# Kernel tuning notes

Measured on AMD Instinct MI355X. Metric: run time of the kernel, lower is better.

## Reference

```python
import jax, jax.numpy as jnp
import numpy as np
from jax import lax

B, T, H, W, E = 64, 8, 8, 8, 512
REC = 2048


def setup_inputs() -> dict:
    key = jax.random.key(0)
    kx, kwi, kwr = jax.random.split(key, 3)
    x = jax.random.normal(kx, (B, T, H, W, E), dtype=jnp.float32)
    W_input = jax.random.normal(kwi, (E, REC), dtype=jnp.float32) / np.sqrt(E)
    W_recurrent = jax.random.normal(kwr, (REC, REC), dtype=jnp.float32) / np.sqrt(REC)
    return {"x": x, "W_input": W_input, "W_recurrent": W_recurrent}


def reference(x, W_input, W_recurrent):
    b, t, h, w, e = x.shape
    R = t * h * w
    rec = W_recurrent.shape[0]
    k = int(rec * 0.4)  # 819, matches torch: int(recurrent_size * 0.4)
    x_seq = jnp.swapaxes(x.reshape(b, R, e), 0, 1)  # [R, B, E]
    row_idx = jnp.arange(b)[:, None]

    def step(r, inp):
        z = r @ W_recurrent                    # [B, REC]
        vals, idx = lax.top_k(z, k)            # [B, k]
        s = jnp.zeros_like(z).at[row_idx, idx].set(vals)  # scatter top-k back
        r_new = jnp.tanh(inp @ W_input + s)
        r_new = r_new / (jnp.linalg.norm(r_new, axis=-1, keepdims=True) + 1e-6)
        return r_new, None

    r0 = jnp.zeros((b, rec), dtype=x.dtype)
    r_final, _ = lax.scan(step, r0, x_seq)
    return r_final
```

## Files before the change

### kernel.cpp

```cpp
#include <hip/hip_runtime.h>

#define NSTEP 512
#define EDIM  512
#define REC   2048
#define NB    64
#define KSEL  819
#define KC    8
#define ZCH   256
#define AP    264
#define CSTR  16896
#define WITC  1048576

typedef unsigned short u16;
typedef __bf16 bf16x8 __attribute__((ext_vector_type(8)));
typedef float  f32x4  __attribute__((ext_vector_type(4)));
typedef unsigned long long ull;

static __device__ __forceinline__ f32x4 mfma16(bf16x8 a, bf16x8 b, f32x4 c) {
    return __builtin_amdgcn_mfma_f32_16x16x32_bf16(a, b, c, 0, 0, 0);
}

static __device__ __forceinline__ void split2(float v, u16& c0, u16& c1) {
    __bf16 b0 = (__bf16)v;
    __bf16 b1 = (__bf16)(v - (float)b0);
    c0 = __builtin_bit_cast(u16, b0);
    c1 = __builtin_bit_cast(u16, b1);
}

static __device__ __forceinline__ void cstore4f(float* p, float v) {
    __hip_atomic_store((unsigned*)p, __float_as_uint(v), __ATOMIC_RELAXED, __HIP_MEMORY_SCOPE_AGENT);
}
static __device__ __forceinline__ void cstore4u(unsigned* p, unsigned v) {
    __hip_atomic_store(p, v, __ATOMIC_RELAXED, __HIP_MEMORY_SCOPE_AGENT);
}
static __device__ __forceinline__ unsigned cload4u(const unsigned* p) {
    return __hip_atomic_load(p, __ATOMIC_RELAXED, __HIP_MEMORY_SCOPE_AGENT);
}
static __device__ __forceinline__ void cstore8u(void* p, ull v) {
    __hip_atomic_store((ull*)p, v, __ATOMIC_RELAXED, __HIP_MEMORY_SCOPE_AGENT);
}
static __device__ __forceinline__ ull cload8u(const void* p) {
    return __hip_atomic_load((const ull*)p, __ATOMIC_RELAXED, __HIP_MEMORY_SCOPE_AGENT);
}
static __device__ __forceinline__ float2 cload8f(const float* p) {
    ull u = cload8u(p);
    float2 v; __builtin_memcpy(&v, &u, 8);
    return v;
}

__device__ __forceinline__ void gbarA(unsigned* bar, int bid, int tid,
                                      unsigned gen, bool wait)
{
    __syncthreads();
    if (tid == 0) cstore4u(&bar[bid], gen);
    if (bid == 0 && tid < 64) {
        const ull* sl = (const ull*)bar;
        for (;;) {
            const ull v0 = cload8u(&sl[tid * 2]);
            const ull v1 = cload8u(&sl[tid * 2 + 1]);
            const bool ok = ((unsigned)v0 >= gen) && ((unsigned)(v0 >> 32) >= gen)
                         && ((unsigned)v1 >= gen) && ((unsigned)(v1 >> 32) >= gen);
            if (__all(ok)) break;
            __builtin_amdgcn_s_sleep(1);
        }
        if (tid < 16) cstore4u(&bar[1024 + tid * 32], gen);
    }
    if (wait) {
        if (tid == 0) {
            const int g = bid >> 4;
            while (cload4u(&bar[1024 + g * 32]) < gen)
                __builtin_amdgcn_s_sleep(1);
            __asm__ volatile("" ::: "memory");
        }
        __syncthreads();
    }
}

__device__ __forceinline__ void gbarB(unsigned* bar, int bid, int tid, unsigned gen)
{
    __syncthreads();
    if (bid < NB && tid == 0) cstore4u(&bar[512 + bid], gen);
    if (bid == 0 && tid < 64) {
        for (;;) {
            const unsigned v = cload4u(&bar[512 + tid]);
            if (__all(v >= gen)) break;
            __builtin_amdgcn_s_sleep(1);
        }
        if (tid < 16) cstore4u(&bar[1536 + tid * 32], gen);
    }
    if (tid == 0) {
        const int g = bid >> 4;
        while (cload4u(&bar[1536 + g * 32]) < gen)
            __builtin_amdgcn_s_sleep(1);
        __asm__ volatile("" ::: "memory");
    }
    __syncthreads();
}

__global__ __launch_bounds__(512, 1)
void rnn_persistent(const float* __restrict__ x, const float* __restrict__ Wi,
                    const float* __restrict__ Wr, float* __restrict__ out,
                    u16* __restrict__ rTu, float* __restrict__ zb,
                    u16* __restrict__ Ybf, u16* __restrict__ WiTu,
                    unsigned* __restrict__ bar)
{
    extern __shared__ __align__(16) char smem[];
    u16* WrSu = (u16*)smem;
    u16* aSu  = (u16*)(smem + 67584);
    float* tp = (float*)smem;
    unsigned*      kS    = (unsigned*)(smem + 67584);
    unsigned char* selS  = (unsigned char*)(smem + 67584 + 8192);
    unsigned*      hist  = (unsigned*)(smem + 67584 + 10240);
    __shared__ unsigned s_byte, s_newrem, s_cnteq;
    __shared__ float red[8];

    const int bid = blockIdx.x;
    const int tid = threadIdx.x;
    const int kc = bid & 7, nc = bid >> 3;
    const int n0 = nc * 64, kcbase = kc * ZCH;
    const int wid = tid >> 6, lane = tid & 63;
    const int q = lane >> 4, l16 = lane & 15;
    const int Moff = (wid & 3) * 16, Npair = wid >> 2;
    const bool isB = (bid < NB);

    {
        const int jt = bid & 31, et = bid >> 5;
        const int j0 = jt * 64, e0 = et * 64;
        const int rr = tid >> 6, ln = tid & 63;
#pragma unroll
        for (int k = 0; k < 8; ++k) {
            const int r = k * 8 + rr;
            tp[r * 65 + ln] = Wi[(long long)(e0 + r) * REC + j0 + ln];
        }
        __syncthreads();
        const int c = tid >> 3, e8 = (tid & 7) * 8;
        u16 h[8], l[8];
#pragma unroll
        for (int i = 0; i < 8; ++i) split2(tp[(e8 + i) * 65 + c], h[i], l[i]);
        ull ph0, ph1, pl0, pl1;
        __builtin_memcpy(&ph0, &h[0], 8); __builtin_memcpy(&ph1, &h[4], 8);
        __builtin_memcpy(&pl0, &l[0], 8); __builtin_memcpy(&pl1, &l[4], 8);
        const long long bI = (long long)(j0 + c) * 512 + e0 + e8;
        cstore8u(&WiTu[bI], ph0);        cstore8u(&WiTu[bI + 4], ph1);
        cstore8u(&WiTu[WITC + bI], pl0); cstore8u(&WiTu[WITC + bI + 4], pl1);
    }
    gbarA(bar, bid, tid, 1u, true);

    {
        const int t0 = bid * 2;
        for (int jc = 0; jc < 32; ++jc) {
            const int j0y = jc * 64;
            f32x4 aY[2][2];
#pragma unroll
            for (int tt = 0; tt < 2; ++tt)
#pragma unroll
                for (int i = 0; i < 2; ++i) aY[tt][i] = (f32x4){0,0,0,0};
            for (int kc2 = 0; kc2 < 2; ++kc2) {
                __syncthreads();
#pragma unroll
                for (int i = 0; i < 8; ++i) {
                    const int chunk = i * 512 + tid;
                    const int cc = chunk >> 11;
                    const int jj = (chunk & 2047) >> 5;
                    const int e8 = chunk & 31;
                    const u16* src = WiTu + (long long)cc * WITC
                                   + (long long)(j0y + jj) * 512 + kc2 * 256 + e8 * 8;
                    const ull w0 = *(const ull*)src;
                    const ull w1 = *(const ull*)(src + 4);
                    u16* dst = WrSu + cc * CSTR + jj * AP + e8 * 8;
                    *(ull*)dst = w0;
                    *(ull*)(dst + 4) = w1;
                }
#pragma unroll
                for (int tt = 0; tt < 2; ++tt) {
                    __syncthreads();
#pragma unroll
                    for (int it = 0; it < 8; ++it) {
                        const int b = it * 8 + wid;
                        const float4 v = *(const float4*)(x
                            + ((long long)b * NSTEP + (t0 + tt)) * EDIM
                            + kc2 * 256 + lane * 4);
                        u16 hh[4], ll[4];
                        split2(v.x, hh[0], ll[0]); split2(v.y, hh[1], ll[1]);
                        split2(v.z, hh[2], ll[2]); split2(v.w, hh[3], ll[3]);
                        ull ph, pl;
                        __builtin_memcpy(&ph, hh, 8); __builtin_memcpy(&pl, ll, 8);
                        *(ull*)&aSu[b * AP + lane * 4] = ph;
                        *(ull*)&aSu[CSTR + b * AP + lane * 4] = pl;
                    }
                    __syncthreads();
                    f32x4 a0 = aY[tt][0], a1 = aY[tt][1];
#pragma unroll
                    for (int ks = 0; ks < 8; ++ks) {
                        const int kk = ks * 32 + q * 8;
                        const u16* ap = aSu + (Moff + l16) * AP + kk;
                        bf16x8 A0 = *(const bf16x8*)(ap);
                        bf16x8 A1 = *(const bf16x8*)(ap + CSTR);
                        const u16* bp0 = WrSu + (Npair * 32 + l16) * AP + kk;
                        bf16x8 B00 = *(const bf16x8*)(bp0);
                        bf16x8 B01 = *(const bf16x8*)(bp0 + CSTR);
                        const u16* bp1 = bp0 + 16 * AP;
                        bf16x8 B10 = *(const bf16x8*)(bp1);
                        bf16x8 B11 = *(const bf16x8*)(bp1 + CSTR);
                        a0 = mfma16(A0, B00, a0);
                        a1 = mfma16(A0, B10, a1);
                        a0 = mfma16(A0, B01, a0);
                        a1 = mfma16(A0, B11, a1);
                        a0 = mfma16(A1, B00, a0);
                        a1 = mfma16(A1, B10, a1);
                    }
                    aY[tt][0] = a0; aY[tt][1] = a1;
                }
            }
            const int jb = j0y + Npair * 32 + l16;
#pragma unroll
            for (int tt = 0; tt < 2; ++tt)
#pragma unroll
                for (int i = 0; i < 4; ++i) {
                    const int row = Moff + q * 4 + i;
                    const unsigned w0 = (unsigned)__builtin_bit_cast(u16, (__bf16)((float*)&aY[tt][0])[i]);
                    const unsigned w1 = (unsigned)__builtin_bit_cast(u16, (__bf16)((float*)&aY[tt][1])[i]);
                    const unsigned o0 = (unsigned)__shfl_xor((int)w0, 1);
                    const unsigned o1 = (unsigned)__shfl_xor((int)w1, 1);
                    if ((lane & 1) == 0) {
                        const long long yb = ((long long)(t0 + tt) * 64 + row) * REC + jb;
                        cstore4u((unsigned*)&Ybf[yb],      w0 | (o0 << 16));
                        cstore4u((unsigned*)&Ybf[yb + 16], w1 | (o1 << 16));
                    }
                }
        }
    }
    {
        const int g = bid * 512 + tid;
        if (g < 65536) cstore8u(rTu + (long long)g * 4, 0ull);
        cstore4f(zb + g, 0.f);
    }
    gbarA(bar, bid, tid, 2u, true);

    {
        for (int it = 0; it < 32; ++it) {
            const int row = it * 8 + wid;
            const int col = lane;
            const float v = Wr[(long long)(kcbase + row) * REC + n0 + col];
            u16 s0, s1; split2(v, s0, s1);
            const int base = col * AP + row;
            WrSu[base] = s0;
            WrSu[CSTR + base] = s1;
        }
        __syncthreads();
    }

    const int hw = tid >> 5, hl = tid & 31;
    for (int t = 0; t < NSTEP; ++t) {
        float* zcur = zb + (size_t)(t & 1) * 131072;
        float* znxt = zb + (size_t)((t + 1) & 1) * 131072;
        cstore4f(znxt + bid * 512 + tid, 0.f);
        {
            ull va[8], vbv[8];
#pragma unroll
            for (int i = 0; i < 8; ++i) {
                const int c = i >> 2;
                const int b = (i & 3) * 16 + hw;
                const u16* src = rTu + (long long)c * 131072 + (long long)b * REC + kcbase + hl * 8;
                va[i] = cload8u(src);
                vbv[i] = cload8u(src + 4);
            }
#pragma unroll
            for (int i = 0; i < 8; ++i) {
                const int c = i >> 2;
                const int b = (i & 3) * 16 + hw;
                u16* dst = aSu + c * CSTR + b * AP + hl * 8;
                *(ull*)dst = va[i];
                *(ull*)(dst + 4) = vbv[i];
            }
        }
        __syncthreads();

        f32x4 acc0 = {0,0,0,0}, acc1 = {0,0,0,0};
#pragma unroll
        for (int ks = 0; ks < 8; ++ks) {
            const int kk = ks * 32 + q * 8;
            const u16* ap = aSu + (Moff + l16) * AP + kk;
            bf16x8 A0 = *(const bf16x8*)(ap);
            bf16x8 A1 = *(const bf16x8*)(ap + CSTR);
            const u16* bp0 = WrSu + (Npair * 32 + l16) * AP + kk;
            bf16x8 B00 = *(const bf16x8*)(bp0);
            bf16x8 B01 = *(const bf16x8*)(bp0 + CSTR);
            const u16* bp1 = bp0 + 16 * AP;
            bf16x8 B10 = *(const bf16x8*)(bp1);
            bf16x8 B11 = *(const bf16x8*)(bp1 + CSTR);
            acc0 = mfma16(A0, B00, acc0);
            acc1 = mfma16(A0, B10, acc1);
            acc0 = mfma16(A0, B01, acc0);
            acc1 = mfma16(A0, B11, acc1);
            acc0 = mfma16(A1, B00, acc0);
            acc1 = mfma16(A1, B10, acc1);
        }
        {
            const int colA = n0 + Npair * 32 + l16;
#pragma unroll
            for (int i = 0; i < 4; ++i) {
                float* zp = zcur + (long long)(Moff + q * 4 + i) * REC + colA;
                unsafeAtomicAdd(zp,      ((float*)&acc0)[i]);
                unsafeAtomicAdd(zp + 16, ((float*)&acc1)[i]);
            }
        }
        ushort4 yv;
        if (isB) yv = *(const ushort4*)&Ybf[((long long)t * 64 + bid) * REC + tid * 4];
        gbarA(bar, bid, tid, (unsigned)(t + 3), isB);

        if (isB) {
            const int b = bid;
            const int j0 = tid * 4;
            float zs[4];
            {
                const float2 u0 = cload8f(zcur + (long long)b * REC + j0);
                const float2 u1 = cload8f(zcur + (long long)b * REC + j0 + 2);
                zs[0] = u0.x; zs[1] = u0.y; zs[2] = u1.x; zs[3] = u1.y;
            }
            unsigned kv[4];
#pragma unroll
            for (int s = 0; s < 4; ++s) {
                const unsigned u = __float_as_uint(zs[s]);
                kv[s] = (u & 0x80000000u) ? ~u : (u | 0x80000000u);
            }
            unsigned* hw_ = hist + wid * 256;
            unsigned prefix = 0, remaining = KSEL;
            int done = 0;
            unsigned char sel[4];
            int sel_set = 0;
            for (int byte = 3; byte >= 0 && !done; --byte) {
                {
                    uint4 zz = {0u, 0u, 0u, 0u};
                    *(uint4*)&hw_[lane * 4] = zz;
                }
                const int shift = byte * 8;
                const unsigned pmask = (byte == 3) ? 0u : (0xFFFFFFFFu << (shift + 8));
#pragma unroll
                for (int s = 0; s < 4; ++s) {
                    if ((kv[s] & pmask) == prefix)
                        atomicAdd(&hw_[(kv[s] >> shift) & 255u], 1u);
                }
                __syncthreads();
                if (tid < 64) {
                    unsigned c0 = 0, c1 = 0, c2 = 0, c3 = 0;
#pragma unroll
                    for (int w = 0; w < 8; ++w) {
                        const uint4 hv = *(const uint4*)&hist[w * 256 + tid * 4];
                        c0 += hv.x; c1 += hv.y; c2 += hv.z; c3 += hv.w;
                    }
                    const unsigned tot = c0 + c1 + c2 + c3;
                    unsigned suf = tot;
#pragma unroll
                    for (int st = 1; st < 64; st <<= 1) {
                        unsigned o = __shfl_down(suf, (unsigned)st);
                        if (tid + st >= 64) o = 0u;
                        suf += o;
                    }
                    unsigned S[5];
                    S[0] = suf; S[1] = suf - c0; S[2] = suf - c0 - c1;
                    S[3] = suf - c0 - c1 - c2; S[4] = suf - tot;
                    const unsigned cc[4] = {c0, c1, c2, c3};
#pragma unroll
                    for (int qq = 0; qq < 4; ++qq) {
                        if (S[qq] >= remaining && S[qq + 1] < remaining) {
                            s_byte = (unsigned)(tid * 4 + qq);
                            s_newrem = remaining - S[qq + 1];
                            s_cnteq = cc[qq];
                        }
                    }
                }
                __syncthreads();
                prefix |= (s_byte << shift);
                remaining = s_newrem;
                if (remaining == s_cnteq) { done = 1; continue; }
                if (s_cnteq <= 64u) {
                    const unsigned maskk = 0xFFFFFFFFu << shift;
                    if (tid == 0) kS[128] = 0u;
                    *(unsigned*)&selS[j0] = 0u;
                    __syncthreads();
#pragma unroll
                    for (int s = 0; s < 4; ++s) {
                        if ((kv[s] & maskk) == prefix) {
                            const unsigned p = atomicAdd(&kS[128], 1u);
                            kS[p] = kv[s];
                            kS[64 + p] = (unsigned)(j0 + s);
                        }
                    }
                    __syncthreads();
                    if (tid < 64) {
                        const unsigned cnt = kS[128];
                        if ((unsigned)lane < cnt) {
                            const unsigned myK = kS[lane];
                            const unsigned myI = kS[64 + lane];
                            unsigned rank = 0;
                            for (unsigned j = 0; j < cnt; ++j) {
                                const unsigned bk = kS[j], bi = kS[64 + j];
                                if (bk > myK || (bk == myK && bi < myI)) ++rank;
                            }
                            if (rank < remaining) selS[myI] = 1;
                        }
                    }
                    __syncthreads();
#pragma unroll
                    for (int s = 0; s < 4; ++s) {
                        const unsigned m = kv[s] & maskk;
                        sel[s] = (m > prefix) ? 1 : ((m == prefix) ? selS[j0 + s] : 0);
                    }
                    sel_set = 1;
                    break;
                }
            }
            if (!sel_set) {
                if (done) {
#pragma unroll
                    for (int s = 0; s < 4; ++s)
                        sel[s] = (kv[s] >= prefix) ? 1 : 0;
                } else {
                    *(uint4*)&kS[j0] = *(uint4*)kv;
                    __syncthreads();
                    if (tid == 0) {
                        unsigned rem = remaining;
                        const unsigned T = prefix;
                        for (int j = 0; j < REC; ++j) {
                            const unsigned k = kS[j];
                            unsigned char sl = 0;
                            if (k > T) sl = 1;
                            else if (k == T && rem > 0u) { sl = 1; --rem; }
                            selS[j] = sl;
                        }
                    }
                    __syncthreads();
#pragma unroll
                    for (int s = 0; s < 4; ++s) sel[s] = selS[j0 + s];
                }
            }
            float rn[4]; float ss = 0.f;
            const u16 ya[4] = {yv.x, yv.y, yv.z, yv.w};
#pragma unroll
            for (int s = 0; s < 4; ++s) {
                const float y = __uint_as_float(((unsigned)ya[s]) << 16);
                const float v = y + (sel[s] ? zs[s] : 0.f);
                const float th = tanhf(v);
                rn[s] = th; ss += th * th;
            }
#pragma unroll
            for (int off = 32; off > 0; off >>= 1)
                ss += __shfl_down(ss, (unsigned)off);
            if (lane == 0) red[wid] = ss;
            __syncthreads();
            float a = 0.f;
#pragma unroll
            for (int i = 0; i < 8; ++i) a += red[i];
            const float inv = 1.0f / (sqrtf(a) + 1e-6f);
            u16 o0[4], o1[4];
            float4 ov;
#pragma unroll
            for (int s = 0; s < 4; ++s) {
                const float v = rn[s] * inv;
                split2(v, o0[s], o1[s]);
                ((float*)&ov)[s] = v;
            }
            ull p0, p1;
            __builtin_memcpy(&p0, o0, 8); __builtin_memcpy(&p1, o1, 8);
            cstore8u(rTu + (long long)b * REC + j0, p0);
            cstore8u(rTu + 131072 + (long long)b * REC + j0, p1);
            if (t == NSTEP - 1)
                *(float4*)&out[(long long)b * REC + j0] = ov;
        }
        gbarB(bar, bid, tid, (unsigned)(t + 1));
    }
}

extern "C" void kernel_launch(void* const* d_in, const int* in_sizes, int n_in,
                              void* d_out, int out_size, void* d_ws, size_t ws_size,
                              hipStream_t stream)
{
    const float* x   = (const float*)d_in[0];
    const float* Win = (const float*)d_in[1];
    const float* Wr  = (const float*)d_in[2];
    float* out = (float*)d_out;

    char* ws = (char*)d_ws;
    const size_t BAR = 8192;
    unsigned* bar  = (unsigned*)ws;
    float*    zb   = (float*)(ws + BAR);
    u16*      rTu  = (u16*)(ws + BAR + 2 * 524288);
    u16*      WiTu = (u16*)(ws + BAR + 2 * 524288 + 524288);
    u16*      Ybf  = (u16*)(ws + BAR + 2 * 524288 + 524288 + 4194304);

    static int smem_set = 0;
    if (!smem_set) {
        hipFuncSetAttribute((const void*)rnn_persistent,
                            hipFuncAttributeMaxDynamicSharedMemorySize, 135168);
        smem_set = 1;
    }
    hipMemsetAsync(bar, 0, BAR, stream);
    rnn_persistent<<<256, 512, 135168, stream>>>(x, Win, Wr, out, rTu, zb, Ybf, WiTu, bar);
}
```

Measured before the change: 7.194 ms.

## Replace flag-array grid barriers with single atomic counter barriers

Replaces the two-level grid barriers with monotonically increasing atomic counters. Previously block 0 polled every block's flag and then broadcast a release to per-group flags. Now each block atomically increments a shared counter and polls it directly, which removes the serial hop through block 0 on every step. The Ybf prefetch load is also moved earlier, ahead of the MFMA loop. The trade-off is atomic contention on one cache line from 256 blocks, plus many pollers hitting the same address.

```diff
diff --git a/kernel.cpp b/kernel.cpp
--- a/kernel.cpp
+++ b/kernel.cpp
@@ -48,50 +48,13 @@
     return v;
 }
 
-__device__ __forceinline__ void gbarA(unsigned* bar, int bid, int tid,
-                                      unsigned gen, bool wait)
-{
+static __device__ __forceinline__ void cbarArrive(unsigned* cnt, int tid) {
     __syncthreads();
-    if (tid == 0) cstore4u(&bar[bid], gen);
-    if (bid == 0 && tid < 64) {
-        const ull* sl = (const ull*)bar;
-        for (;;) {
-            const ull v0 = cload8u(&sl[tid * 2]);
-            const ull v1 = cload8u(&sl[tid * 2 + 1]);
-            const bool ok = ((unsigned)v0 >= gen) && ((unsigned)(v0 >> 32) >= gen)
-                         && ((unsigned)v1 >= gen) && ((unsigned)(v1 >> 32) >= gen);
-            if (__all(ok)) break;
-            __builtin_amdgcn_s_sleep(1);
-        }
-        if (tid < 16) cstore4u(&bar[1024 + tid * 32], gen);
-    }
-    if (wait) {
-        if (tid == 0) {
-            const int g = bid >> 4;
-            while (cload4u(&bar[1024 + g * 32]) < gen)
-                __builtin_amdgcn_s_sleep(1);
-            __asm__ volatile("" ::: "memory");
-        }
-        __syncthreads();
-    }
-}
-
-__device__ __forceinline__ void gbarB(unsigned* bar, int bid, int tid, unsigned gen)
-{
-    __syncthreads();
-    if (bid < NB && tid == 0) cstore4u(&bar[512 + bid], gen);
-    if (bid == 0 && tid < 64) {
-        for (;;) {
-            const unsigned v = cload4u(&bar[512 + tid]);
-            if (__all(v >= gen)) break;
-            __builtin_amdgcn_s_sleep(1);
-        }
-        if (tid < 16) cstore4u(&bar[1536 + tid * 32], gen);
-    }
+    if (tid == 0) atomicAdd(cnt, 1u);
+}
+static __device__ __forceinline__ void cbarWait(unsigned* cnt, int tid, unsigned target) {
     if (tid == 0) {
-        const int g = bid >> 4;
-        while (cload4u(&bar[1536 + g * 32]) < gen)
-            __builtin_amdgcn_s_sleep(1);
+        while (cload4u(cnt) < target) __builtin_amdgcn_s_sleep(1);
         __asm__ volatile("" ::: "memory");
     }
     __syncthreads();
@@ -122,6 +85,8 @@
     const int q = lane >> 4, l16 = lane & 15;
     const int Moff = (wid & 3) * 16, Npair = wid >> 2;
     const bool isB = (bid < NB);
+    unsigned* cntA = &bar[0];
+    unsigned* cntB = &bar[32];
 
     {
         const int jt = bid & 31, et = bid >> 5;
@@ -144,7 +109,8 @@
         cstore8u(&WiTu[bI], ph0);        cstore8u(&WiTu[bI + 4], ph1);
         cstore8u(&WiTu[WITC + bI], pl0); cstore8u(&WiTu[WITC + bI + 4], pl1);
     }
-    gbarA(bar, bid, tid, 1u, true);
+    cbarArrive(cntA, tid);
+    cbarWait(cntA, tid, 256u * 1u);
 
     {
         const int t0 = bid * 2;
@@ -235,7 +201,8 @@
         if (g < 65536) cstore8u(rTu + (long long)g * 4, 0ull);
         cstore4f(zb + g, 0.f);
     }
-    gbarA(bar, bid, tid, 2u, true);
+    cbarArrive(cntA, tid);
+    cbarWait(cntA, tid, 256u * 2u);
 
     {
         for (int it = 0; it < 32; ++it) {
@@ -275,6 +242,9 @@
             }
         }
         __syncthreads();
+
+        ushort4 yv;
+        if (isB) yv = *(const ushort4*)&Ybf[((long long)t * 64 + bid) * REC + tid * 4];
 
         f32x4 acc0 = {0,0,0,0}, acc1 = {0,0,0,0};
 #pragma unroll
@@ -305,9 +275,8 @@
                 unsafeAtomicAdd(zp + 16, ((float*)&acc1)[i]);
             }
         }
-        ushort4 yv;
-        if (isB) yv = *(const ushort4*)&Ybf[((long long)t * 64 + bid) * REC + tid * 4];
-        gbarA(bar, bid, tid, (unsigned)(t + 3), isB);
+        cbarArrive(cntA, tid);
+        if (isB) cbarWait(cntA, tid, 256u * (unsigned)(t + 3));
 
         if (isB) {
             const int b = bid;
@@ -468,7 +437,9 @@
             if (t == NSTEP - 1)
                 *(float4*)&out[(long long)b * REC + j0] = ov;
         }
-        gbarB(bar, bid, tid, (unsigned)(t + 1));
+        __syncthreads();
+        if (isB && tid == 0) atomicAdd(cntB, 1u);
+        cbarWait(cntB, tid, 64u * (unsigned)(t + 1));
     }
 }
 
```

New measurement: 9.832 ms. 36.7% more time.
